# Kernel optimization log

Hardware: AMD Instinct MI355X
Metric: run time of the kernel (lower is better)

The kernel has to match this reference:

```python
import jax, jax.numpy as jnp
import numpy as np

N_OPT, OUT_F, IN_F = 16, 1024, 1024
B, A = 8, 512


def setup_inputs() -> dict:
    key = jax.random.key(0)
    k1, k2, k3, k4 = jax.random.split(key, 4)
    x = jax.random.normal(k1, (B, A, IN_F), dtype=jnp.float32)
    sp = jax.random.uniform(k2, (B, N_OPT), dtype=jnp.float32)
    selection_probs = sp / jnp.sum(sp, axis=-1, keepdims=True)
    # kaiming-uniform-ish init scale
    bound_w = 1.0 / np.sqrt(IN_F)
    weight = jax.random.uniform(k3, (N_OPT, OUT_F, IN_F), dtype=jnp.float32,
                                minval=-bound_w, maxval=bound_w)
    bias = jax.random.uniform(k4, (N_OPT, OUT_F), dtype=jnp.float32,
                              minval=-bound_w, maxval=bound_w)
    return {"x": x, "selection_probs": selection_probs, "weight": weight, "bias": bias}


def reference(x, selection_probs, weight, bias):
    # Math identical to torch forward:
    #   transformed = einsum('nij,baj->bani', weight, x)
    #   out = einsum('bani,bn->bai', transformed, selection_probs)
    # reassociated efficiently: mix weights per-example first, then one batched matmul.
    w_mixed = jnp.einsum('nij,bn->bij', weight, selection_probs)   # [B, out, in]
    out = jnp.einsum('bij,baj->bai', w_mixed, x)                   # [B, A, out]
    b_mixed = jnp.einsum('ni,bn->bi', bias, selection_probs)       # [B, out]
    return out + b_mixed[:, None, :]
```

## Files before the change

### kernel.cpp

```cpp
#include <hip/hip_runtime.h>
#include <hip/hip_bf16.h>


#define B_SZ 8
#define A_SZ 512
#define IN_F 1024
#define OUT_F 1024
#define N_OPT 16

typedef short short8 __attribute__((ext_vector_type(8)));
typedef float floatx4 __attribute__((ext_vector_type(4)));

__device__ __forceinline__ unsigned short f2bf(float f) {
    unsigned int u = __builtin_bit_cast(unsigned int, f);
    u += 0x7fffu + ((u >> 16) & 1u);
    return (unsigned short)(u >> 16);
}

#define GLOBAL_LOAD_LDS16(g, l)                                                    \
    __builtin_amdgcn_global_load_lds(                                              \
        (const __attribute__((address_space(1))) void*)(g),                        \
        (__attribute__((address_space(3))) void*)(l), 16, 0, 0)

__global__ __launch_bounds__(256) void selin_prep(
    const float* __restrict__ x, const float* __restrict__ sp,
    const float* __restrict__ weight, const float* __restrict__ bias,
    unsigned short* __restrict__ wm, unsigned short* __restrict__ xbf,
    float* __restrict__ bmixed)
{
    const int bid = blockIdx.x;
    const int tid = threadIdx.x;

    if (bid < 1024) {
        __shared__ float sps[B_SZ * N_OPT];
        if (tid < B_SZ * N_OPT) sps[tid] = sp[tid];
        __syncthreads();
        const int e4 = bid * 256 + tid;
        const float4* w4 = (const float4*)weight;
        float4 w[N_OPT];
#pragma unroll
        for (int n = 0; n < N_OPT; n++)
            w[n] = w4[(size_t)n * (IN_F * OUT_F / 4) + e4];
#pragma unroll
        for (int b = 0; b < B_SZ; b++) {
            float ax = 0.f, ay = 0.f, az = 0.f, aw = 0.f;
#pragma unroll
            for (int n = 0; n < N_OPT; n++) {
                float s = sps[b * N_OPT + n];
                ax += s * w[n].x; ay += s * w[n].y;
                az += s * w[n].z; aw += s * w[n].w;
            }
            ushort4 o = make_ushort4(f2bf(ax), f2bf(ay), f2bf(az), f2bf(aw));
            ((ushort4*)wm)[(size_t)b * (IN_F * OUT_F / 4) + e4] = o;
        }
#pragma unroll
        for (int j = 0; j < 4; j++) {
            const int idx = bid * 1024 + j * 256 + tid;
            float4 v = ((const float4*)x)[idx];
            ((ushort4*)xbf)[idx] =
                make_ushort4(f2bf(v.x), f2bf(v.y), f2bf(v.z), f2bf(v.w));
        }
    } else {
        __shared__ float sps[B_SZ * N_OPT];
        if (tid < B_SZ * N_OPT) sps[tid] = sp[tid];
        __syncthreads();
        const int idx = (bid - 1024) * 256 + tid;
        const int b = idx >> 8, i4 = idx & 255;
        const float4* bias4 = (const float4*)bias;
        float ax = 0.f, ay = 0.f, az = 0.f, aw = 0.f;
#pragma unroll
        for (int n = 0; n < N_OPT; n++) {
            float s = sps[b * N_OPT + n];
            float4 v = bias4[n * 256 + i4];
            ax += s * v.x; ay += s * v.y; az += s * v.z; aw += s * v.w;
        }
        ((float4*)bmixed)[idx] = make_float4(ax, ay, az, aw);
    }
}

__global__ __launch_bounds__(256) void selin_gemm(
    const unsigned short* __restrict__ xbf, const unsigned short* __restrict__ wm,
    const float* __restrict__ bmixed, float* __restrict__ out)
{
    __shared__ __align__(16) unsigned short As[2][64 * 32];
    __shared__ __align__(16) unsigned short Bs[2][64 * 32];

    const int tid = threadIdx.x;
    const int bid = blockIdx.x;
    const int b   = bid & 7;
    const int t   = bid >> 3;
    const int mb  = t & 7;
    const int nb  = t >> 3;
    const int m0  = mb * 64, n0 = nb * 64;

    const unsigned short* Ag = xbf + ((size_t)b * A_SZ  + m0) * IN_F;
    const unsigned short* Bg = wm  + ((size_t)b * OUT_F + n0) * IN_F;

    const int ga = (tid >> 2) * IN_F + (tid & 3) * 8;

    const int lane = tid & 63;
    const int wv   = tid >> 6;
    const int wmi  = wv >> 1, wni = wv & 1;
    const int lm   = lane & 15, kq = lane >> 4;

    floatx4 acc[2][2];
#pragma unroll
    for (int i = 0; i < 2; i++)
#pragma unroll
        for (int j = 0; j < 2; j++)
            acc[i][j] = (floatx4){0.f, 0.f, 0.f, 0.f};

    for (int k0 = 0; k0 < IN_F; k0 += 64) {
        GLOBAL_LOAD_LDS16(Ag + ga + k0,      &As[0][tid * 8]);
        GLOBAL_LOAD_LDS16(Ag + ga + k0 + 32, &As[1][tid * 8]);
        GLOBAL_LOAD_LDS16(Bg + ga + k0,      &Bs[0][tid * 8]);
        GLOBAL_LOAD_LDS16(Bg + ga + k0 + 32, &Bs[1][tid * 8]);
        __syncthreads();

#pragma unroll
        for (int kh = 0; kh < 2; kh++) {
            short8 a[2], bb[2];
#pragma unroll
            for (int mi = 0; mi < 2; mi++)
                a[mi] = *(const short8*)&As[kh][(wmi * 32 + mi * 16 + lm) * 32 + kq * 8];
#pragma unroll
            for (int ni = 0; ni < 2; ni++)
                bb[ni] = *(const short8*)&Bs[kh][(wni * 32 + ni * 16 + lm) * 32 + kq * 8];

#pragma unroll
            for (int mi = 0; mi < 2; mi++)
#pragma unroll
                for (int ni = 0; ni < 2; ni++)
                    acc[mi][ni] = __builtin_amdgcn_mfma_f32_16x16x32_bf16(
                        a[mi], bb[ni], acc[mi][ni], 0, 0, 0);
        }
        __syncthreads();
    }

#pragma unroll
    for (int ni = 0; ni < 2; ni++) {
        const int gcol = n0 + wni * 32 + ni * 16 + lm;
        const float bv = bmixed[b * OUT_F + gcol];
#pragma unroll
        for (int mi = 0; mi < 2; mi++) {
            const int grow = m0 + wmi * 32 + mi * 16 + kq * 4;
            float* op = out + ((size_t)b * A_SZ + grow) * OUT_F + gcol;
#pragma unroll
            for (int r = 0; r < 4; r++)
                op[(size_t)r * OUT_F] = acc[mi][ni][r] + bv;
        }
    }
}

extern "C" void kernel_launch(void* const* d_in, const int* in_sizes, int n_in,
                              void* d_out, int out_size, void* d_ws, size_t ws_size,
                              hipStream_t stream) {
    const float* x      = (const float*)d_in[0];
    const float* sp     = (const float*)d_in[1];
    const float* weight = (const float*)d_in[2];
    const float* bias   = (const float*)d_in[3];
    float* out = (float*)d_out;

    unsigned short* wm  = (unsigned short*)d_ws;
    unsigned short* xbf = wm + (size_t)B_SZ * OUT_F * IN_F;
    float* bmixed       = (float*)(xbf + (size_t)B_SZ * A_SZ * IN_F);

    selin_prep<<<1032, 256, 0, stream>>>(x, sp, weight, bias, wm, xbf, bmixed);
    selin_gemm<<<1024, 256, 0, stream>>>(xbf, wm, bmixed, out);
}
```

Measured before the change: 130.4 us.

## Enlarge GEMM tile to 128x64 and double-buffer LDS staging

```diff
diff --git a/kernel.cpp b/kernel.cpp
--- a/kernel.cpp
+++ b/kernel.cpp
@@ -82,16 +82,15 @@
     const unsigned short* __restrict__ xbf, const unsigned short* __restrict__ wm,
     const float* __restrict__ bmixed, float* __restrict__ out)
 {
-    __shared__ __align__(16) unsigned short As[2][64 * 32];
-    __shared__ __align__(16) unsigned short Bs[2][64 * 32];
+    __shared__ __align__(16) unsigned short As[2][2][128 * 32];
+    __shared__ __align__(16) unsigned short Bs[2][2][64 * 32];
 
     const int tid = threadIdx.x;
     const int bid = blockIdx.x;
     const int b   = bid & 7;
-    const int t   = bid >> 3;
-    const int mb  = t & 7;
-    const int nb  = t >> 3;
-    const int m0  = mb * 64, n0 = nb * 64;
+    const int tb  = bid >> 3;
+    const int m0  = (tb & 3) * 128;
+    const int n0  = (tb >> 2) * 64;
 
     const unsigned short* Ag = xbf + ((size_t)b * A_SZ  + m0) * IN_F;
     const unsigned short* Bg = wm  + ((size_t)b * OUT_F + n0) * IN_F;
@@ -103,47 +102,59 @@
     const int wmi  = wv >> 1, wni = wv & 1;
     const int lm   = lane & 15, kq = lane >> 4;
 
-    floatx4 acc[2][2];
+    floatx4 acc[4][2];
 #pragma unroll
-    for (int i = 0; i < 2; i++)
+    for (int i = 0; i < 4; i++)
 #pragma unroll
         for (int j = 0; j < 2; j++)
             acc[i][j] = (floatx4){0.f, 0.f, 0.f, 0.f};
 
-    for (int k0 = 0; k0 < IN_F; k0 += 64) {
-        GLOBAL_LOAD_LDS16(Ag + ga + k0,      &As[0][tid * 8]);
-        GLOBAL_LOAD_LDS16(Ag + ga + k0 + 32, &As[1][tid * 8]);
-        GLOBAL_LOAD_LDS16(Bg + ga + k0,      &Bs[0][tid * 8]);
-        GLOBAL_LOAD_LDS16(Bg + ga + k0 + 32, &Bs[1][tid * 8]);
-        __syncthreads();
+    auto stage = [&](int d, int kg) {
+        GLOBAL_LOAD_LDS16(Ag + ga + kg,                  &As[d][0][tid * 8]);
+        GLOBAL_LOAD_LDS16(Ag + ga + 64 * IN_F + kg,      &As[d][0][2048 + tid * 8]);
+        GLOBAL_LOAD_LDS16(Ag + ga + kg + 32,             &As[d][1][tid * 8]);
+        GLOBAL_LOAD_LDS16(Ag + ga + 64 * IN_F + kg + 32, &As[d][1][2048 + tid * 8]);
+        GLOBAL_LOAD_LDS16(Bg + ga + kg,                  &Bs[d][0][tid * 8]);
+        GLOBAL_LOAD_LDS16(Bg + ga + kg + 32,             &Bs[d][1][tid * 8]);
+    };
 
+    auto compute = [&](int c) {
 #pragma unroll
         for (int kh = 0; kh < 2; kh++) {
-            short8 a[2], bb[2];
+            short8 a[4], bb[2];
 #pragma unroll
-            for (int mi = 0; mi < 2; mi++)
-                a[mi] = *(const short8*)&As[kh][(wmi * 32 + mi * 16 + lm) * 32 + kq * 8];
+            for (int mi = 0; mi < 4; mi++)
+                a[mi] = *(const short8*)&As[c][kh][(wmi * 64 + mi * 16 + lm) * 32 + kq * 8];
 #pragma unroll
             for (int ni = 0; ni < 2; ni++)
-                bb[ni] = *(const short8*)&Bs[kh][(wni * 32 + ni * 16 + lm) * 32 + kq * 8];
-
+                bb[ni] = *(const short8*)&Bs[c][kh][(wni * 32 + ni * 16 + lm) * 32 + kq * 8];
 #pragma unroll
-            for (int mi = 0; mi < 2; mi++)
+            for (int mi = 0; mi < 4; mi++)
 #pragma unroll
                 for (int ni = 0; ni < 2; ni++)
                     acc[mi][ni] = __builtin_amdgcn_mfma_f32_16x16x32_bf16(
                         a[mi], bb[ni], acc[mi][ni], 0, 0, 0);
         }
+    };
+
+    stage(0, 0);
+    __syncthreads();
+    int cur = 0;
+    for (int ks = 1; ks < 16; ++ks) {
+        stage(cur ^ 1, ks * 64);
+        compute(cur);
         __syncthreads();
+        cur ^= 1;
     }
+    compute(cur);
 
 #pragma unroll
     for (int ni = 0; ni < 2; ni++) {
         const int gcol = n0 + wni * 32 + ni * 16 + lm;
         const float bv = bmixed[b * OUT_F + gcol];
 #pragma unroll
-        for (int mi = 0; mi < 2; mi++) {
-            const int grow = m0 + wmi * 32 + mi * 16 + kq * 4;
+        for (int mi = 0; mi < 4; mi++) {
+            const int grow = m0 + wmi * 64 + mi * 16 + kq * 4;
             float* op = out + ((size_t)b * A_SZ + grow) * OUT_F + gcol;
 #pragma unroll
             for (int r = 0; r < 4; r++)
@@ -166,5 +177,5 @@
     float* bmixed       = (float*)(xbf + (size_t)B_SZ * A_SZ * IN_F);
 
     selin_prep<<<1032, 256, 0, stream>>>(x, sp, weight, bias, wm, xbf, bmixed);
-    selin_gemm<<<1024, 256, 0, stream>>>(xbf, wm, bmixed, out);
+    selin_gemm<<<512, 256, 0, stream>>>(xbf, wm, bmixed, out);
 }
```

Result: no change. 132.5 us (+1.6%).
